# Performance work log

Hardware: AMD Instinct MI355X
Metric: run time of the kernel (lower is better)

Reference implementation:

```python
import jax, jax.numpy as jnp
import numpy as np

N_NODES, N_EDGES = 50000, 800000
IN_DIM, HID_DIM, OUT_DIM = 512, 256, 256


def setup_inputs() -> dict:
    key = jax.random.key(0)
    ks = jax.random.split(key, 8)
    x = jax.random.normal(ks[0], (N_NODES, IN_DIM), dtype=jnp.float32)
    edge_index = jax.random.randint(ks[1], (2, N_EDGES), 0, N_NODES, dtype=jnp.int64)
    # GCNConv lin weights (no bias in lin; separate additive bias after aggregation)
    W1 = jax.random.normal(ks[2], (IN_DIM, HID_DIM), dtype=jnp.float32) * (1.0 / np.sqrt(IN_DIM))
    b1 = jnp.zeros((HID_DIM,), dtype=jnp.float32)
    W2 = jax.random.normal(ks[3], (HID_DIM, OUT_DIM), dtype=jnp.float32) * (1.0 / np.sqrt(HID_DIM))
    b2 = jnp.zeros((OUT_DIM,), dtype=jnp.float32)
    # projection head nn.Linear(out_dim, out_dim)
    Wp = jax.random.normal(ks[4], (OUT_DIM, OUT_DIM), dtype=jnp.float32) * (1.0 / np.sqrt(OUT_DIM))
    bp = jnp.zeros((OUT_DIM,), dtype=jnp.float32)
    return {"x": x, "edge_index": edge_index, "W1": W1, "b1": b1,
            "W2": W2, "b2": b2, "Wp": Wp, "bp": bp}


def _gcn_conv(x, W, b, src, dst, n):
    # x' = D^{-1/2}(A+I)D^{-1/2} (x W) + b ; deg includes self-loop (+1)
    h = x @ W  # [N, F]
    deg = jax.ops.segment_sum(jnp.ones(src.shape[0], h.dtype), dst, num_segments=n) + 1.0
    dis = jax.lax.rsqrt(deg)  # deg^{-1/2}, [N]
    msg = (dis[src] * dis[dst])[:, None] * h[src]  # [E, F] gathered+scaled messages
    agg = jax.ops.segment_sum(msg, dst, num_segments=n)  # scatter-add to dst
    # self-loop contribution: norm = dis[i]^2, message = h[i]
    return agg + (dis * dis)[:, None] * h + b


def reference(x, edge_index, W1, b1, W2, b2, Wp, bp):
    src, dst = edge_index[0], edge_index[1]
    n = x.shape[0]
    h = jax.nn.relu(_gcn_conv(x, W1, b1, src, dst, n))
    # eval mode: dropout is identity
    h = _gcn_conv(h, W2, b2, src, dst, n)
    return h @ Wp + bp
```

## Files before the change

### kernel.cpp

```cpp
#include <hip/hip_runtime.h>
#include <hip/hip_bf16.h>

typedef __bf16 bf16_8 __attribute__((ext_vector_type(8)));
typedef float  f32_4  __attribute__((ext_vector_type(4)));

#define NNODES 50000
#define NEDGES 800000
#define INDIM  512
#define HIDDIM 256
#define CSTRIDE 264

__device__ inline void gload_lds16(const __hip_bfloat16* g, __hip_bfloat16* l) {
    __builtin_amdgcn_global_load_lds(
        (const __attribute__((address_space(1))) void*)g,
        (__attribute__((address_space(3))) void*)l, 16, 0, 0);
}


__global__ void zero_kernel(int* p, int n) {
    int i = blockIdx.x * 256 + threadIdx.x;
    if (i < n) p[i] = 0;
}

__global__ void detect_kernel(const int* __restrict__ ei,
                              const unsigned short* __restrict__ xh,
                              int* __restrict__ flags) {
    int t = threadIdx.x;
    unsigned long long nz = __ballot(ei[1 + 2 * t] != 0);
    unsigned e = (xh[2 * t] >> 7) & 0xFF;
    unsigned long long ok = __ballot(e >= 90 && e <= 142);
    if (t == 0) {
        flags[0] = (nz == 0ull) ? 1 : 0;
        flags[1] = (__popcll(ok) >= 48) ? 1 : 0;
    }
}

__global__ void count_kernel(const int* __restrict__ idx, const int* __restrict__ flags,
                             int* __restrict__ deg, int E) {
    int e = blockIdx.x * 256 + threadIdx.x;
    if (e >= E) return;
    int d = flags[0] ? idx[2 * (E + e)] : idx[E + e];
    d = min(max(d, 0), NNODES - 1);
    atomicAdd(&deg[d], 1);
}

__global__ void reduce_kernel(const int* __restrict__ deg, int* __restrict__ bsum, int n) {
    __shared__ int l[256];
    int i = blockIdx.x * 256 + threadIdx.x;
    l[threadIdx.x] = (i < n) ? deg[i] : 0;
    __syncthreads();
    for (int o = 128; o > 0; o >>= 1) {
        if (threadIdx.x < o) l[threadIdx.x] += l[threadIdx.x + o];
        __syncthreads();
    }
    if (threadIdx.x == 0) bsum[blockIdx.x] = l[0];
}

__global__ void scanb_kernel(const int* __restrict__ bsum, int nb,
                             int* __restrict__ boff, int* __restrict__ offs_last) {
    __shared__ int l[256];
    int v = (threadIdx.x < nb) ? bsum[threadIdx.x] : 0;
    l[threadIdx.x] = v;
    __syncthreads();
    for (int o = 1; o < 256; o <<= 1) {
        int t = (threadIdx.x >= o) ? l[threadIdx.x - o] : 0;
        __syncthreads();
        l[threadIdx.x] += t;
        __syncthreads();
    }
    if (threadIdx.x < nb) boff[threadIdx.x] = l[threadIdx.x] - v;
    if (threadIdx.x == 255) *offs_last = l[255];
}

__global__ void local_scan_kernel(const int* __restrict__ deg, const int* __restrict__ boff,
                                  int* __restrict__ offs, float* __restrict__ dis, int n) {
    __shared__ int l[256];
    int i = blockIdx.x * 256 + threadIdx.x;
    int v = (i < n) ? deg[i] : 0;
    l[threadIdx.x] = v;
    __syncthreads();
    for (int o = 1; o < 256; o <<= 1) {
        int t = (threadIdx.x >= o) ? l[threadIdx.x - o] : 0;
        __syncthreads();
        l[threadIdx.x] += t;
        __syncthreads();
    }
    if (i < n) {
        offs[i] = boff[blockIdx.x] + l[threadIdx.x] - v;
        dis[i]  = rsqrtf((float)v + 1.0f);
    }
}

__global__ void fill_kernel(const int* __restrict__ idx, const int* __restrict__ flags,
                            const int* __restrict__ offs, int* __restrict__ cursor,
                            int* __restrict__ csr, int E) {
    int e = blockIdx.x * 256 + threadIdx.x;
    if (e >= E) return;
    int s, d;
    if (flags[0]) { s = idx[2 * e]; d = idx[2 * (E + e)]; }
    else          { s = idx[e];     d = idx[E + e]; }
    s = min(max(s, 0), NNODES - 1);
    d = min(max(d, 0), NNODES - 1);
    int p = atomicAdd(&cursor[d], 1);
    csr[offs[d] + p] = s;
}

__global__ void wf_kernel(const void* __restrict__ W2v, const void* __restrict__ Wpv,
                          const void* __restrict__ b2v, const void* __restrict__ bpv,
                          const int* __restrict__ flags,
                          void* __restrict__ Wfv, void* __restrict__ bfv) {
    const bool bf = flags[1] != 0;
    const int r = blockIdx.x;
    const int c = threadIdx.x;
    float acc = 0.0f;
    for (int k = 0; k < HIDDIM; ++k) {
        float a = (r < HIDDIM)
            ? (bf ? (float)((const __hip_bfloat16*)W2v)[(size_t)r * HIDDIM + k]
                  : ((const float*)W2v)[(size_t)r * HIDDIM + k])
            : (bf ? (float)((const __hip_bfloat16*)b2v)[k]
                  : ((const float*)b2v)[k]);
        float b = bf ? (float)((const __hip_bfloat16*)Wpv)[(size_t)k * HIDDIM + c]
                     : ((const float*)Wpv)[(size_t)k * HIDDIM + c];
        acc += a * b;
    }
    if (r < HIDDIM) {
        if (bf) ((__hip_bfloat16*)Wfv)[(size_t)r * HIDDIM + c] = (__hip_bfloat16)acc;
        else    ((float*)Wfv)[(size_t)r * HIDDIM + c] = acc;
    } else {
        acc += bf ? (float)((const __hip_bfloat16*)bpv)[c] : ((const float*)bpv)[c];
        if (bf) ((__hip_bfloat16*)bfv)[c] = (__hip_bfloat16)acc;
        else    ((float*)bfv)[c] = acc;
    }
}

__global__ void repack_kernel(const void* __restrict__ Wv, const int* __restrict__ flags,
                              __hip_bfloat16* __restrict__ P, int K, int N) {
    int ntiles = N / 16;
    int nt = blockIdx.x % ntiles;
    int kt = blockIdx.x / ntiles;
    int lane = threadIdx.x;
    int quad = lane >> 4, l16 = lane & 15;
    size_t pbase = ((size_t)blockIdx.x * 64 + lane) * 8;
    int k0 = kt * 32 + quad * 8;
    int col = nt * 16 + l16;
    bool bf = flags[1] != 0;
    for (int j = 0; j < 8; ++j) {
        size_t src = (size_t)(k0 + j) * N + col;
        P[pbase + j] = bf ? ((const __hip_bfloat16*)Wv)[src]
                          : (__hip_bfloat16)((const float*)Wv)[src];
    }
}

template<int K, bool ABF>
__device__ __forceinline__ void gemm_loop(const void* __restrict__ Av,
                                          const __hip_bfloat16* __restrict__ Bp,
                                          __hip_bfloat16* smem, f32_4 (&acc)[16],
                                          int wave, int lane, int row0, bool active) {
    constexpr int NKB = K / 32;
    const int quad = lane >> 4;
    const int l16  = lane & 15;
    __hip_bfloat16* buf0 = smem;
    __hip_bfloat16* buf1 = smem + 8192;
    const size_t arowK = (size_t)(active ? row0 + l16 : l16) * K;

    bf16_8 afr[3];

    auto stage = [&](int s) {
        const __hip_bfloat16* slab = Bp + (size_t)s * 8192;
        __hip_bfloat16* buf = (s & 1) ? buf1 : buf0;
        #pragma unroll
        for (int i = 0; i < 4; ++i) {
            int ch = wave * 4 + i;
            gload_lds16(slab + ch * 512 + lane * 8, buf + ch * 512);
        }
    };
    auto loadA = [&](int s) -> bf16_8 {
        return *(const bf16_8*)((const __hip_bfloat16*)Av + arowK + (size_t)s * 32 + quad * 8);
    };
    auto loadA32 = [&](int s) -> bf16_8 {
        const float* Af = (const float*)Av + arowK + (size_t)s * 32 + quad * 8;
        f32_4 lo = *(const f32_4*)Af;
        f32_4 hi = *(const f32_4*)(Af + 4);
        bf16_8 r;
        #pragma unroll
        for (int j = 0; j < 4; ++j) { r[j] = (__bf16)lo[j]; r[j + 4] = (__bf16)hi[j]; }
        return r;
    };

    if constexpr (ABF) afr[0] = loadA(0);
    stage(0);
    if constexpr (ABF) afr[1] = loadA(1);
    stage(1);

    #pragma unroll
    for (int s = 0; s < NKB; ++s) {
        if (s + 1 < NKB) {
            if constexpr (ABF) asm volatile("s_waitcnt vmcnt(5)" ::: "memory");
            else               asm volatile("s_waitcnt vmcnt(4)" ::: "memory");
        } else {
            asm volatile("s_waitcnt vmcnt(0)" ::: "memory");
        }
        __builtin_amdgcn_sched_barrier(0);
        __builtin_amdgcn_s_barrier();
        __builtin_amdgcn_sched_barrier(0);
        if (ABF && s + 2 < NKB) afr[(s + 2) % 3] = loadA(s + 2);
        bf16_8 a;
        if constexpr (ABF) a = afr[s % 3];
        else               a = loadA32(s);
        if (active) {
            const __hip_bfloat16* bb = ((s & 1) ? buf1 : buf0) + lane * 8;
            #pragma unroll
            for (int ct = 0; ct < 16; ++ct) {
                bf16_8 b = *(const bf16_8*)(bb + ct * 512);
                acc[ct] = __builtin_amdgcn_mfma_f32_16x16x32_bf16(a, b, acc[ct], 0, 0, 0);
            }
        }
        __builtin_amdgcn_sched_barrier(0);
        asm volatile("s_waitcnt lgkmcnt(0)" ::: "memory");
        __builtin_amdgcn_sched_barrier(0);
        __builtin_amdgcn_s_barrier();
        __builtin_amdgcn_sched_barrier(0);
        if (s + 2 < NKB) stage(s + 2);
    }
}

template<int K>
__global__ __launch_bounds__(256, 4)
void gemm_kernel(const void* __restrict__ Av,
                 const void* __restrict__ Av_alt,
                 const __hip_bfloat16* __restrict__ Bp,
                 const void* __restrict__ biasv,
                 void* __restrict__ Cv,
                 const int* __restrict__ flags, int amode, int cmode, int M) {
    constexpr int N = 256;
    __shared__ __align__(16) __hip_bfloat16 smem[16896];

    const int wave = threadIdx.x >> 6;
    const int lane = threadIdx.x & 63;
    const int quad = lane >> 4;
    const int l16  = lane & 15;
    const int row0 = blockIdx.x * 64 + wave * 16;
    const bool active = row0 < M;
    const bool bf  = flags[1] != 0;
    const bool abf = amode || bf;
    const bool cbf = cmode || bf;
    const void* A = (bf || !Av_alt) ? Av : Av_alt;

    f32_4 acc[16] = {};
    if (abf) gemm_loop<K, true >(A, Bp, smem, acc, wave, lane, row0, active);
    else     gemm_loop<K, false>(A, Bp, smem, acc, wave, lane, row0, active);

    if (cbf) {
        __hip_bfloat16* cs = smem + wave * 16 * CSTRIDE;
        if (active) {
            #pragma unroll
            for (int ct = 0; ct < 16; ++ct) {
                int col = ct * 16 + l16;
                float bv = 0.0f;
                if (biasv) bv = bf ? (float)((const __hip_bfloat16*)biasv)[col]
                                   : ((const float*)biasv)[col];
                #pragma unroll
                for (int rr = 0; rr < 4; ++rr)
                    cs[(quad * 4 + rr) * CSTRIDE + col] = (__hip_bfloat16)(acc[ct][rr] + bv);
            }
            const int rh = lane >> 5;
            const int ce = (lane & 31) * 8;
            #pragma unroll
            for (int pass = 0; pass < 8; ++pass) {
                int r = pass * 2 + rh;
                __hip_bfloat16* crow = (__hip_bfloat16*)Cv + (size_t)(row0 + r) * N;
                *(bf16_8*)(crow + ce) = *(const bf16_8*)(cs + r * CSTRIDE + ce);
            }
        }
    } else if (active) {
        #pragma unroll
        for (int ct = 0; ct < 16; ++ct) {
            int col = ct * 16 + l16;
            float bv = 0.0f;
            if (biasv) bv = bf ? (float)((const __hip_bfloat16*)biasv)[col]
                               : ((const float*)biasv)[col];
            #pragma unroll
            for (int rr = 0; rr < 4; ++rr) {
                int row = row0 + quad * 4 + rr;
                ((float*)Cv)[(size_t)row * N + col] = acc[ct][rr] + bv;
            }
        }
    }
}

__device__ inline void acc_row(f32_4& a0, f32_4& a1, float w, bf16_8 r) {
    a0[0] += w * (float)r[0]; a0[1] += w * (float)r[1];
    a0[2] += w * (float)r[2]; a0[3] += w * (float)r[3];
    a1[0] += w * (float)r[4]; a1[1] += w * (float)r[5];
    a1[2] += w * (float)r[6]; a1[3] += w * (float)r[7];
}

__global__ __launch_bounds__(256)
void agg_kernel(const __hip_bfloat16* __restrict__ h,
                const int* __restrict__ csr,
                const int* __restrict__ offs,
                const float* __restrict__ dis,
                const void* __restrict__ biasv,
                const int* __restrict__ flags,
                __hip_bfloat16* __restrict__ out,
                __hip_bfloat16* __restrict__ out_alt,
                int relu) {
    const int wave = threadIdx.x >> 6;
    const int lane = threadIdx.x & 63;
    const int n = blockIdx.x * 4 + wave;
    if (n >= NNODES) return;
    const int half = lane >> 5;
    const int l32  = lane & 31;
    __hip_bfloat16* o = (flags[1] || !out_alt) ? out : out_alt;

    const float dn = dis[n];
    const int beg = offs[n], end = offs[n + 1];
    f32_4 a0 = {}, a1 = {};

    int j = beg + half;
    for (; j + 2 < end; j += 4) {
        int sa = csr[j], sb = csr[j + 2];
        bf16_8 ra = *(const bf16_8*)(h + (size_t)sa * HIDDIM + l32 * 8);
        bf16_8 rb = *(const bf16_8*)(h + (size_t)sb * HIDDIM + l32 * 8);
        float wa = dis[sa], wb = dis[sb];
        acc_row(a0, a1, wa, ra);
        acc_row(a0, a1, wb, rb);
    }
    if (j < end) {
        int sa = csr[j];
        bf16_8 ra = *(const bf16_8*)(h + (size_t)sa * HIDDIM + l32 * 8);
        acc_row(a0, a1, dis[sa], ra);
    }

    #pragma unroll
    for (int k = 0; k < 4; ++k) {
        a0[k] += __shfl_xor(a0[k], 32);
        a1[k] += __shfl_xor(a1[k], 32);
    }

    bf16_8 rn = *(const bf16_8*)(h + (size_t)n * HIDDIM + l32 * 8);
    float bv[8] = {0, 0, 0, 0, 0, 0, 0, 0};
    if (biasv) {
        if (flags[1]) {
            bf16_8 bb = ((const bf16_8*)biasv)[l32];
            #pragma unroll
            for (int k = 0; k < 8; ++k) bv[k] = (float)bb[k];
        } else {
            f32_4 blo = *((const f32_4*)biasv + 2 * l32);
            f32_4 bhi = *((const f32_4*)biasv + 2 * l32 + 1);
            #pragma unroll
            for (int k = 0; k < 4; ++k) { bv[k] = blo[k]; bv[k + 4] = bhi[k]; }
        }
    }
    const float dn2 = dn * dn;
    float v[8];
    #pragma unroll
    for (int k = 0; k < 4; ++k) {
        v[k]     = dn * a0[k] + dn2 * (float)rn[k]     + bv[k];
        v[k + 4] = dn * a1[k] + dn2 * (float)rn[k + 4] + bv[k + 4];
    }
    if (relu) {
        #pragma unroll
        for (int k = 0; k < 8; ++k) v[k] = fmaxf(v[k], 0.0f);
    }
    if (half == 0) {
        bf16_8 ov;
        #pragma unroll
        for (int k = 0; k < 8; ++k) ov[k] = (__bf16)v[k];
        *(bf16_8*)(o + (size_t)n * HIDDIM + l32 * 8) = ov;
    }
}


extern "C" void kernel_launch(void* const* d_in, const int* in_sizes, int n_in,
                              void* d_out, int out_size, void* d_ws, size_t ws_size,
                              hipStream_t stream) {
    const int M = NNODES, E = NEDGES;
    const void* x  = d_in[0];
    const int*  ei = (const int*)d_in[1];
    const void* W1 = d_in[2];
    const void* b1 = d_in[3];
    const void* W2 = d_in[4];
    const void* b2 = d_in[5];
    const void* Wp = d_in[6];
    const void* bp = d_in[7];

    char* w = (char*)d_ws;
    size_t off = 0;
    auto alloc = [&](size_t bytes) -> void* {
        void* p = w + off;
        off += (bytes + 255) & ~(size_t)255;
        return p;
    };
    int*   deg    = (int*)alloc((size_t)M * 4);
    int*   cursor = (int*)alloc((size_t)M * 4);
    int*   offs   = (int*)alloc((size_t)(M + 1) * 4);
    float* dis    = (float*)alloc((size_t)M * 4);
    int*   flags  = (int*)alloc(256);
    int*   bsum   = (int*)alloc(256 * 4);
    int*   boff   = (int*)alloc(256 * 4);
    int*   csr    = (int*)alloc((size_t)E * 4);
    __hip_bfloat16* W1p = (__hip_bfloat16*)alloc((size_t)INDIM * HIDDIM * 2);
    __hip_bfloat16* Wfp = (__hip_bfloat16*)alloc((size_t)HIDDIM * HIDDIM * 2);
    void* Wf  = alloc((size_t)HIDDIM * HIDDIM * 4);
    void* bfu = alloc((size_t)HIDDIM * 4);
    if (ws_size < off) return;

    __hip_bfloat16* h  = (__hip_bfloat16*)d_out;
    __hip_bfloat16* ha = (__hip_bfloat16*)d_in[0];
    __hip_bfloat16* g_alt = (__hip_bfloat16*)((char*)d_in[0] + (size_t)M * INDIM * 4 / 2);

    const int nb = (M + 255) / 256;

    zero_kernel<<<nb, 256, 0, stream>>>(deg, M);
    zero_kernel<<<nb, 256, 0, stream>>>(cursor, M);
    detect_kernel<<<1, 64, 0, stream>>>(ei, (const unsigned short*)x, flags);
    count_kernel<<<(E + 255) / 256, 256, 0, stream>>>(ei, flags, deg, E);
    reduce_kernel<<<nb, 256, 0, stream>>>(deg, bsum, M);
    scanb_kernel<<<1, 256, 0, stream>>>(bsum, nb, boff, &offs[M]);
    local_scan_kernel<<<nb, 256, 0, stream>>>(deg, boff, offs, dis, M);
    fill_kernel<<<(E + 255) / 256, 256, 0, stream>>>(ei, flags, offs, cursor, csr, E);

    wf_kernel<<<HIDDIM + 1, HIDDIM, 0, stream>>>(W2, Wp, b2, bp, flags, Wf, bfu);
    repack_kernel<<<(INDIM / 32) * (HIDDIM / 16), 64, 0, stream>>>(W1, flags, W1p, INDIM, HIDDIM);
    repack_kernel<<<(HIDDIM / 32) * (HIDDIM / 16), 64, 0, stream>>>(Wf, flags, Wfp, HIDDIM, HIDDIM);

    const int ggrid = (M + 63) / 64;
    const int agrid = (M + 3) / 4;

    gemm_kernel<INDIM><<<ggrid, 256, 0, stream>>>(x, nullptr, W1p, nullptr, h, flags, 0, 1, M);
    agg_kernel<<<agrid, 256, 0, stream>>>(h, csr, offs, dis, b1, flags, ha, nullptr, 1);

    agg_kernel<<<agrid, 256, 0, stream>>>(ha, csr, offs, dis, nullptr, flags, h, g_alt, 0);
    gemm_kernel<HIDDIM><<<ggrid, 256, 0, stream>>>(h, g_alt, Wfp, bfu, d_out, flags, 1, 0, M);
}
```

Measured before the change: 505.0 us.

## Prefetch fp32 A tiles two stages ahead and tile the weight-fusion kernel

The fp32 path of the GEMM main loop now issues its A-operand loads two k-stages ahead into a 3-slot register ring, like the bf16 path, and converts them to bf16 only when they are used. This hides global load latency that was previously exposed on each iteration of the first-layer GEMM over the fp32 input. The vmcnt threshold is raised from 4 to 6 to cover the two extra outstanding loads. Separately, the W2·Wp fusion kernel computes 8 rows per block with W2 rows staged in LDS, cutting the launch to 33 blocks. The ring costs more registers under the 4-blocks-per-CU launch bound.

```diff
diff --git a/kernel.cpp b/kernel.cpp
--- a/kernel.cpp
+++ b/kernel.cpp
@@ -105,28 +105,46 @@
     csr[offs[d] + p] = s;
 }
 
-__global__ void wf_kernel(const void* __restrict__ W2v, const void* __restrict__ Wpv,
-                          const void* __restrict__ b2v, const void* __restrict__ bpv,
-                          const int* __restrict__ flags,
-                          void* __restrict__ Wfv, void* __restrict__ bfv) {
+__global__ __launch_bounds__(256)
+void wf_kernel(const void* __restrict__ W2v, const void* __restrict__ Wpv,
+               const void* __restrict__ b2v, const void* __restrict__ bpv,
+               const int* __restrict__ flags,
+               void* __restrict__ Wfv, void* __restrict__ bfv) {
     const bool bf = flags[1] != 0;
-    const int r = blockIdx.x;
     const int c = threadIdx.x;
-    float acc = 0.0f;
-    for (int k = 0; k < HIDDIM; ++k) {
-        float a = (r < HIDDIM)
-            ? (bf ? (float)((const __hip_bfloat16*)W2v)[(size_t)r * HIDDIM + k]
-                  : ((const float*)W2v)[(size_t)r * HIDDIM + k])
-            : (bf ? (float)((const __hip_bfloat16*)b2v)[k]
-                  : ((const float*)b2v)[k]);
-        float b = bf ? (float)((const __hip_bfloat16*)Wpv)[(size_t)k * HIDDIM + c]
-                     : ((const float*)Wpv)[(size_t)k * HIDDIM + c];
-        acc += a * b;
-    }
-    if (r < HIDDIM) {
-        if (bf) ((__hip_bfloat16*)Wfv)[(size_t)r * HIDDIM + c] = (__hip_bfloat16)acc;
-        else    ((float*)Wfv)[(size_t)r * HIDDIM + c] = acc;
+    if (blockIdx.x < 32) {
+        __shared__ float As[8 * 256];
+        const int r0 = blockIdx.x * 8;
+        #pragma unroll
+        for (int i = 0; i < 8; ++i) {
+            int idx = i * 256 + c;
+            int r = idx >> 8, k = idx & 255;
+            As[idx] = bf ? (float)((const __hip_bfloat16*)W2v)[(size_t)(r0 + r) * HIDDIM + k]
+                         : ((const float*)W2v)[(size_t)(r0 + r) * HIDDIM + k];
+        }
+        __syncthreads();
+        float acc[8] = {};
+        #pragma unroll 8
+        for (int k = 0; k < HIDDIM; ++k) {
+            float b = bf ? (float)((const __hip_bfloat16*)Wpv)[(size_t)k * HIDDIM + c]
+                         : ((const float*)Wpv)[(size_t)k * HIDDIM + c];
+            #pragma unroll
+            for (int r = 0; r < 8; ++r) acc[r] += As[r * 256 + k] * b;
+        }
+        #pragma unroll
+        for (int r = 0; r < 8; ++r) {
+            if (bf) ((__hip_bfloat16*)Wfv)[(size_t)(r0 + r) * HIDDIM + c] = (__hip_bfloat16)acc[r];
+            else    ((float*)Wfv)[(size_t)(r0 + r) * HIDDIM + c] = acc[r];
+        }
     } else {
+        float acc = 0.0f;
+        #pragma unroll 8
+        for (int k = 0; k < HIDDIM; ++k) {
+            float a = bf ? (float)((const __hip_bfloat16*)b2v)[k] : ((const float*)b2v)[k];
+            float b = bf ? (float)((const __hip_bfloat16*)Wpv)[(size_t)k * HIDDIM + c]
+                         : ((const float*)Wpv)[(size_t)k * HIDDIM + c];
+            acc += a * b;
+        }
         acc += bf ? (float)((const __hip_bfloat16*)bpv)[c] : ((const float*)bpv)[c];
         if (bf) ((__hip_bfloat16*)bfv)[c] = (__hip_bfloat16)acc;
         else    ((float*)bfv)[c] = acc;
@@ -157,6 +175,7 @@
                                           __hip_bfloat16* smem, f32_4 (&acc)[16],
                                           int wave, int lane, int row0, bool active) {
     constexpr int NKB = K / 32;
+    constexpr int BVM = ABF ? 5 : 6;
     const int quad = lane >> 4;
     const int l16  = lane & 15;
     __hip_bfloat16* buf0 = smem;
@@ -164,6 +183,7 @@
     const size_t arowK = (size_t)(active ? row0 + l16 : l16) * K;
 
     bf16_8 afr[3];
+    f32_4  alo[3], ahi[3];
 
     auto stage = [&](int s) {
         const __hip_bfloat16* slab = Bp + (size_t)s * 8192;
@@ -177,36 +197,40 @@
     auto loadA = [&](int s) -> bf16_8 {
         return *(const bf16_8*)((const __hip_bfloat16*)Av + arowK + (size_t)s * 32 + quad * 8);
     };
-    auto loadA32 = [&](int s) -> bf16_8 {
+    auto loadA32 = [&](int s, int slot) {
         const float* Af = (const float*)Av + arowK + (size_t)s * 32 + quad * 8;
-        f32_4 lo = *(const f32_4*)Af;
-        f32_4 hi = *(const f32_4*)(Af + 4);
-        bf16_8 r;
-        #pragma unroll
-        for (int j = 0; j < 4; ++j) { r[j] = (__bf16)lo[j]; r[j + 4] = (__bf16)hi[j]; }
-        return r;
+        alo[slot] = *(const f32_4*)Af;
+        ahi[slot] = *(const f32_4*)(Af + 4);
     };
 
-    if constexpr (ABF) afr[0] = loadA(0);
+    if constexpr (ABF) afr[0] = loadA(0); else loadA32(0, 0);
     stage(0);
-    if constexpr (ABF) afr[1] = loadA(1);
+    if constexpr (ABF) afr[1] = loadA(1); else loadA32(1, 1);
     stage(1);
 
     #pragma unroll
     for (int s = 0; s < NKB; ++s) {
         if (s + 1 < NKB) {
             if constexpr (ABF) asm volatile("s_waitcnt vmcnt(5)" ::: "memory");
-            else               asm volatile("s_waitcnt vmcnt(4)" ::: "memory");
+            else               asm volatile("s_waitcnt vmcnt(6)" ::: "memory");
         } else {
             asm volatile("s_waitcnt vmcnt(0)" ::: "memory");
         }
         __builtin_amdgcn_sched_barrier(0);
         __builtin_amdgcn_s_barrier();
         __builtin_amdgcn_sched_barrier(0);
-        if (ABF && s + 2 < NKB) afr[(s + 2) % 3] = loadA(s + 2);
+        if (s + 2 < NKB) {
+            if constexpr (ABF) afr[(s + 2) % 3] = loadA(s + 2);
+            else               loadA32(s + 2, (s + 2) % 3);
+        }
         bf16_8 a;
-        if constexpr (ABF) a = afr[s % 3];
-        else               a = loadA32(s);
+        if constexpr (ABF) {
+            a = afr[s % 3];
+        } else {
+            const int sl = s % 3;
+            #pragma unroll
+            for (int j = 0; j < 4; ++j) { a[j] = (__bf16)alo[sl][j]; a[j + 4] = (__bf16)ahi[sl][j]; }
+        }
         if (active) {
             const __hip_bfloat16* bb = ((s & 1) ? buf1 : buf0) + lane * 8;
             #pragma unroll
@@ -222,6 +246,7 @@
         __builtin_amdgcn_sched_barrier(0);
         if (s + 2 < NKB) stage(s + 2);
     }
+    (void)BVM;
 }
 
 template<int K>
@@ -421,7 +446,7 @@
     local_scan_kernel<<<nb, 256, 0, stream>>>(deg, boff, offs, dis, M);
     fill_kernel<<<(E + 255) / 256, 256, 0, stream>>>(ei, flags, offs, cursor, csr, E);
 
-    wf_kernel<<<HIDDIM + 1, HIDDIM, 0, stream>>>(W2, Wp, b2, bp, flags, Wf, bfu);
+    wf_kernel<<<33, 256, 0, stream>>>(W2, Wp, b2, bp, flags, Wf, bfu);
     repack_kernel<<<(INDIM / 32) * (HIDDIM / 16), 64, 0, stream>>>(W1, flags, W1p, INDIM, HIDDIM);
     repack_kernel<<<(HIDDIM / 32) * (HIDDIM / 16), 64, 0, stream>>>(Wf, flags, Wfp, HIDDIM, HIDDIM);
 
```

After: 455.7 us. 1.11x faster.
